# Kernel tuning notes

Measured on AMD Instinct MI355X. Metric: run time of the kernel, lower is better.

Reference implementation:

```python
import jax, jax.numpy as jnp
import numpy as np

EPS = 1e-6  # torch F.pairwise_distance adds eps to the difference


def setup_inputs() -> dict:
    key = jax.random.key(0)
    k1, k2 = jax.random.split(key)
    n_nodes, d = 50000, 512
    n_edges = 150000
    z = jax.random.normal(k1, (n_nodes, d), dtype=jnp.float32)
    edge_index = jax.random.randint(k2, (2, n_edges), 0, n_nodes, dtype=jnp.int64)
    return {"z": z, "edge_index": edge_index}


def reference(z, edge_index):
    # gather endpoint embeddings: [n_edges, d]
    a = z[edge_index[0]]
    b = z[edge_index[1]]
    # row-normalize to unit L2 norm (matches _norm_batch)
    a = a / jnp.linalg.norm(a, axis=1, keepdims=True)
    b = b / jnp.linalg.norm(b, axis=1, keepdims=True)
    # pairwise L2 distance with torch's eps offset
    diff = a - b + EPS
    distance = jnp.sqrt(jnp.sum(diff * diff, axis=1))
    value = 1.0 - distance
    return jax.nn.sigmoid(value)
```

## Files before the change

### kernel.cpp

```cpp
#include <hip/hip_runtime.h>
#include <hip/hip_fp16.h>
#include <hip/hip_fp8.h>
#include <math.h>

#define EPS 1e-6f

typedef float floatx2_t __attribute__((ext_vector_type(2)));

template <bool HI>
static __device__ __forceinline__ unsigned int pack2_fp8(float a, float b,
                                                         unsigned int old) {
#if __has_builtin(__builtin_amdgcn_cvt_pk_fp8_f32)
    return (unsigned int)__builtin_amdgcn_cvt_pk_fp8_f32(a, b, (int)old, HI);
#else
    __hip_fp8x2_e4m3 h(float2{a, b});
    unsigned int v = (unsigned int)h.__x;
    return HI ? ((old & 0x0000FFFFu) | (v << 16)) : ((old & 0xFFFF0000u) | v);
#endif
}

template <bool HI>
static __device__ __forceinline__ float2 unpack2_fp8(unsigned int w) {
#if __has_builtin(__builtin_amdgcn_cvt_pk_f32_fp8)
    floatx2_t f = __builtin_amdgcn_cvt_pk_f32_fp8((int)w, HI);
    return make_float2(f.x, f.y);
#else
    __hip_fp8x2_e4m3 h;
    h.__x = (__hip_fp8x2_storage_t)(HI ? (w >> 16) : (w & 0xFFFFu));
    float2 r = (float2)h;
    return r;
#endif
}

__global__ __launch_bounds__(256) void prep_fp8_kernel(
    const float* __restrict__ z, unsigned int* __restrict__ zq, int n_nodes) {
    const int lane = threadIdx.x & 63;
    const int wid = (blockIdx.x * 256 + threadIdx.x) >> 6;
    const int n0 = wid * 2;
    const int n1 = n0 + 1;
    if (n0 >= n_nodes) return;
    const bool has1 = (n1 < n_nodes);

    const float4* r0 = (const float4*)(z + (size_t)n0 * 512);
    const float4* r1 = (const float4*)(z + (size_t)(has1 ? n1 : n0) * 512);
    float4 p0 = r0[lane];
    float4 q0 = r0[lane + 64];
    float4 p1 = r1[lane];
    float4 q1 = r1[lane + 64];

    float s2a = p0.x*p0.x + p0.y*p0.y + p0.z*p0.z + p0.w*p0.w
              + q0.x*q0.x + q0.y*q0.y + q0.z*q0.z + q0.w*q0.w;
    float s2b = p1.x*p1.x + p1.y*p1.y + p1.z*p1.z + p1.w*p1.w
              + q1.x*q1.x + q1.y*q1.y + q1.z*q1.z + q1.w*q1.w;

    #pragma unroll
    for (int off = 32; off > 0; off >>= 1) {
        s2a += __shfl_xor(s2a, off, 64);
        s2b += __shfl_xor(s2b, off, 64);
    }
    const float rna = 1.0f / sqrtf(s2a);
    const float rnb = 1.0f / sqrtf(s2b);

    {
        unsigned int u0 = pack2_fp8<false>(p0.x * rna, p0.y * rna, 0u);
        u0 = pack2_fp8<true>(p0.z * rna, p0.w * rna, u0);
        unsigned int u1 = pack2_fp8<false>(q0.x * rna, q0.y * rna, 0u);
        u1 = pack2_fp8<true>(q0.z * rna, q0.w * rna, u1);
        ((uint2*)(zq + (size_t)n0 * 128))[lane] = make_uint2(u0, u1);
    }
    if (has1) {
        unsigned int u0 = pack2_fp8<false>(p1.x * rnb, p1.y * rnb, 0u);
        u0 = pack2_fp8<true>(p1.z * rnb, p1.w * rnb, u0);
        unsigned int u1 = pack2_fp8<false>(q1.x * rnb, q1.y * rnb, 0u);
        u1 = pack2_fp8<true>(q1.z * rnb, q1.w * rnb, u1);
        ((uint2*)(zq + (size_t)n1 * 128))[lane] = make_uint2(u0, u1);
    }
}

__global__ __launch_bounds__(256) void edge_fp8_kernel(
    const unsigned int* __restrict__ zq, const int* __restrict__ edge_index,
    float* __restrict__ out, int n_edges) {
    const int lane = threadIdx.x & 63;
    const int wid = (blockIdx.x * 256 + threadIdx.x) >> 6;
    const int e0 = wid * 4;
    if (e0 >= n_edges) return;
    const int valid = min(n_edges - e0, 4);

    int s[4], d[4];
    #pragma unroll
    for (int k = 0; k < 4; ++k) {
        int e = e0 + ((k < valid) ? k : 0);
        s[k] = edge_index[e];
        d[k] = edge_index[e + n_edges];
    }

    uint2 av[4], bv[4];
    #pragma unroll
    for (int k = 0; k < 4; ++k) {
        av[k] = ((const uint2*)(zq + (size_t)s[k] * 128))[lane];
        bv[k] = ((const uint2*)(zq + (size_t)d[k] * 128))[lane];
    }

    float dot[4];
    #pragma unroll
    for (int k = 0; k < 4; ++k) {
        float2 a01 = unpack2_fp8<false>(av[k].x);
        float2 a23 = unpack2_fp8<true>(av[k].x);
        float2 a45 = unpack2_fp8<false>(av[k].y);
        float2 a67 = unpack2_fp8<true>(av[k].y);
        float2 b01 = unpack2_fp8<false>(bv[k].x);
        float2 b23 = unpack2_fp8<true>(bv[k].x);
        float2 b45 = unpack2_fp8<false>(bv[k].y);
        float2 b67 = unpack2_fp8<true>(bv[k].y);
        float t = fmaf(a01.x, b01.x, 0.0f);
        t = fmaf(a01.y, b01.y, t);
        t = fmaf(a23.x, b23.x, t);
        t = fmaf(a23.y, b23.y, t);
        t = fmaf(a45.x, b45.x, t);
        t = fmaf(a45.y, b45.y, t);
        t = fmaf(a67.x, b67.x, t);
        t = fmaf(a67.y, b67.y, t);
        dot[k] = t;
    }

    #pragma unroll
    for (int off = 32; off > 0; off >>= 1) {
        #pragma unroll
        for (int k = 0; k < 4; ++k) dot[k] += __shfl_xor(dot[k], off, 64);
    }

    if (lane == 0) {
        const float self_val = 1.0f - sqrtf(512.0f) * EPS;
        float o[4];
        #pragma unroll
        for (int k = 0; k < 4; ++k) {
            float v;
            if (s[k] == d[k]) {
                v = self_val;
            } else {
                float t = fmaxf(2.0f - 2.0f * dot[k], 0.0f);
                v = 1.0f - sqrtf(t);
            }
            o[k] = 1.0f / (1.0f + expf(-v));
        }
        if (valid == 4) {
            ((float4*)(out + e0))[0] = make_float4(o[0], o[1], o[2], o[3]);
        } else {
            for (int k = 0; k < valid; ++k) out[e0 + k] = o[k];
        }
    }
}

__global__ __launch_bounds__(256) void node_rnorm_kernel(
    const float* __restrict__ z, float* __restrict__ rnorm, int n_nodes) {
    const int lane = threadIdx.x & 63;
    const int node = blockIdx.x * 4 + (threadIdx.x >> 6);
    if (node >= n_nodes) return;
    const float4* row = (const float4*)(z + (size_t)node * 512);
    float4 p = row[lane];
    float4 q = row[lane + 64];
    float s = p.x*p.x + p.y*p.y + p.z*p.z + p.w*p.w
            + q.x*q.x + q.y*q.y + q.z*q.z + q.w*q.w;
    #pragma unroll
    for (int off = 32; off > 0; off >>= 1) s += __shfl_down(s, off, 64);
    if (lane == 0) rnorm[node] = 1.0f / sqrtf(s);
}

__global__ __launch_bounds__(256) void edge_dist_kernel(
    const float* __restrict__ z, const int* __restrict__ edge_index,
    const float* __restrict__ rnorm, float* __restrict__ out, int n_edges) {
    const int lane = threadIdx.x & 63;
    const int edge = blockIdx.x * 4 + (threadIdx.x >> 6);
    if (edge >= n_edges) return;
    const int src = edge_index[edge];
    const int dst = edge_index[edge + n_edges];
    const float rna = rnorm[src];
    const float rnb = rnorm[dst];
    const float4* ra = (const float4*)(z + (size_t)src * 512);
    const float4* rb = (const float4*)(z + (size_t)dst * 512);
    float4 a0 = ra[lane];
    float4 b0 = rb[lane];
    float4 a1 = ra[lane + 64];
    float4 b1 = rb[lane + 64];
    float sacc = 0.0f;
    #define ACC(ac, bc) { float dv = (ac) * rna - (bc) * rnb + EPS; sacc = fmaf(dv, dv, sacc); }
    ACC(a0.x, b0.x) ACC(a0.y, b0.y) ACC(a0.z, b0.z) ACC(a0.w, b0.w)
    ACC(a1.x, b1.x) ACC(a1.y, b1.y) ACC(a1.z, b1.z) ACC(a1.w, b1.w)
    #undef ACC
    #pragma unroll
    for (int off = 32; off > 0; off >>= 1) sacc += __shfl_down(sacc, off, 64);
    if (lane == 0) {
        float value = 1.0f - sqrtf(sacc);
        out[edge] = 1.0f / (1.0f + expf(-value));
    }
}

extern "C" void kernel_launch(void* const* d_in, const int* in_sizes, int n_in,
                              void* d_out, int out_size, void* d_ws, size_t ws_size,
                              hipStream_t stream) {
    const float* z = (const float*)d_in[0];
    const int* edge_index = (const int*)d_in[1];
    float* out = (float*)d_out;

    const int n_nodes = in_sizes[0] / 512;
    const int n_edges = in_sizes[1] / 2;

    const size_t zq_bytes = (size_t)n_nodes * 512;

    if (ws_size >= zq_bytes) {
        unsigned int* zq = (unsigned int*)d_ws;
        {
            int waves = (n_nodes + 1) / 2;
            int blocks = (waves + 3) / 4;
            prep_fp8_kernel<<<blocks, 256, 0, stream>>>(z, zq, n_nodes);
        }
        {
            int waves = (n_edges + 3) / 4;
            int blocks = (waves + 3) / 4;
            edge_fp8_kernel<<<blocks, 256, 0, stream>>>(zq, edge_index, out, n_edges);
        }
    } else {
        float* rnorm = (float*)d_ws;
        {
            int blocks = (n_nodes + 3) / 4;
            node_rnorm_kernel<<<blocks, 256, 0, stream>>>(z, rnorm, n_nodes);
        }
        {
            int blocks = (n_edges + 3) / 4;
            edge_dist_kernel<<<blocks, 256, 0, stream>>>(z, edge_index, rnorm, out, n_edges);
        }
    }
}
```

Before: 172.1 us.

## Process eight edges per wavefront with 8-lane groups and 16-byte fp8 loads

The edge kernel now assigns an 8-lane group to each edge, so one wavefront handles eight edges. Each lane issues four 16-byte loads per endpoint row instead of one 8-byte load, and the reduction needs only three shuffle steps. The prep kernel handles four nodes per wavefront instead of two, which gives more memory parallelism per wave. The cost is more registers per lane and smaller contiguous chunks per row access.

```diff
diff --git a/kernel.cpp b/kernel.cpp
--- a/kernel.cpp
+++ b/kernel.cpp
@@ -32,48 +32,61 @@
 #endif
 }
 
+static __device__ __forceinline__ float dot_u4_fp8(uint4 a, uint4 b, float t) {
+    #pragma unroll
+    for (int j = 0; j < 4; ++j) {
+        unsigned int aw = (&a.x)[j];
+        unsigned int bw = (&b.x)[j];
+        float2 alo = unpack2_fp8<false>(aw);
+        float2 ahi = unpack2_fp8<true>(aw);
+        float2 blo = unpack2_fp8<false>(bw);
+        float2 bhi = unpack2_fp8<true>(bw);
+        t = fmaf(alo.x, blo.x, t);
+        t = fmaf(alo.y, blo.y, t);
+        t = fmaf(ahi.x, bhi.x, t);
+        t = fmaf(ahi.y, bhi.y, t);
+    }
+    return t;
+}
+
 __global__ __launch_bounds__(256) void prep_fp8_kernel(
     const float* __restrict__ z, unsigned int* __restrict__ zq, int n_nodes) {
     const int lane = threadIdx.x & 63;
     const int wid = (blockIdx.x * 256 + threadIdx.x) >> 6;
-    const int n0 = wid * 2;
-    const int n1 = n0 + 1;
+    const int n0 = wid * 4;
     if (n0 >= n_nodes) return;
-    const bool has1 = (n1 < n_nodes);
-
-    const float4* r0 = (const float4*)(z + (size_t)n0 * 512);
-    const float4* r1 = (const float4*)(z + (size_t)(has1 ? n1 : n0) * 512);
-    float4 p0 = r0[lane];
-    float4 q0 = r0[lane + 64];
-    float4 p1 = r1[lane];
-    float4 q1 = r1[lane + 64];
-
-    float s2a = p0.x*p0.x + p0.y*p0.y + p0.z*p0.z + p0.w*p0.w
-              + q0.x*q0.x + q0.y*q0.y + q0.z*q0.z + q0.w*q0.w;
-    float s2b = p1.x*p1.x + p1.y*p1.y + p1.z*p1.z + p1.w*p1.w
-              + q1.x*q1.x + q1.y*q1.y + q1.z*q1.z + q1.w*q1.w;
-
+
+    int n[4];
+    float4 p[4], q[4];
+    #pragma unroll
+    for (int k = 0; k < 4; ++k) {
+        n[k] = min(n0 + k, n_nodes - 1);
+        const float4* r = (const float4*)(z + (size_t)n[k] * 512);
+        p[k] = r[lane];
+        q[k] = r[lane + 64];
+    }
+
+    float s2[4];
+    #pragma unroll
+    for (int k = 0; k < 4; ++k) {
+        s2[k] = p[k].x*p[k].x + p[k].y*p[k].y + p[k].z*p[k].z + p[k].w*p[k].w
+              + q[k].x*q[k].x + q[k].y*q[k].y + q[k].z*q[k].z + q[k].w*q[k].w;
+    }
     #pragma unroll
     for (int off = 32; off > 0; off >>= 1) {
-        s2a += __shfl_xor(s2a, off, 64);
-        s2b += __shfl_xor(s2b, off, 64);
-    }
-    const float rna = 1.0f / sqrtf(s2a);
-    const float rnb = 1.0f / sqrtf(s2b);
-
-    {
-        unsigned int u0 = pack2_fp8<false>(p0.x * rna, p0.y * rna, 0u);
-        u0 = pack2_fp8<true>(p0.z * rna, p0.w * rna, u0);
-        unsigned int u1 = pack2_fp8<false>(q0.x * rna, q0.y * rna, 0u);
-        u1 = pack2_fp8<true>(q0.z * rna, q0.w * rna, u1);
-        ((uint2*)(zq + (size_t)n0 * 128))[lane] = make_uint2(u0, u1);
-    }
-    if (has1) {
-        unsigned int u0 = pack2_fp8<false>(p1.x * rnb, p1.y * rnb, 0u);
-        u0 = pack2_fp8<true>(p1.z * rnb, p1.w * rnb, u0);
-        unsigned int u1 = pack2_fp8<false>(q1.x * rnb, q1.y * rnb, 0u);
-        u1 = pack2_fp8<true>(q1.z * rnb, q1.w * rnb, u1);
-        ((uint2*)(zq + (size_t)n1 * 128))[lane] = make_uint2(u0, u1);
+        #pragma unroll
+        for (int k = 0; k < 4; ++k) s2[k] += __shfl_xor(s2[k], off, 64);
+    }
+
+    #pragma unroll
+    for (int k = 0; k < 4; ++k) {
+        if (k > 0 && n0 + k >= n_nodes) break;
+        const float rn = 1.0f / sqrtf(s2[k]);
+        unsigned int u0 = pack2_fp8<false>(p[k].x * rn, p[k].y * rn, 0u);
+        u0 = pack2_fp8<true>(p[k].z * rn, p[k].w * rn, u0);
+        unsigned int u1 = pack2_fp8<false>(q[k].x * rn, q[k].y * rn, 0u);
+        u1 = pack2_fp8<true>(q[k].z * rn, q[k].w * rn, u1);
+        ((uint2*)(zq + (size_t)n[k] * 128))[lane] = make_uint2(u0, u1);
     }
 }
 
@@ -81,73 +94,47 @@
     const unsigned int* __restrict__ zq, const int* __restrict__ edge_index,
     float* __restrict__ out, int n_edges) {
     const int lane = threadIdx.x & 63;
+    const int t = lane & 7;
+    const int g = lane >> 3;
     const int wid = (blockIdx.x * 256 + threadIdx.x) >> 6;
-    const int e0 = wid * 4;
-    if (e0 >= n_edges) return;
-    const int valid = min(n_edges - e0, 4);
-
-    int s[4], d[4];
-    #pragma unroll
-    for (int k = 0; k < 4; ++k) {
-        int e = e0 + ((k < valid) ? k : 0);
-        s[k] = edge_index[e];
-        d[k] = edge_index[e + n_edges];
-    }
-
-    uint2 av[4], bv[4];
-    #pragma unroll
-    for (int k = 0; k < 4; ++k) {
-        av[k] = ((const uint2*)(zq + (size_t)s[k] * 128))[lane];
-        bv[k] = ((const uint2*)(zq + (size_t)d[k] * 128))[lane];
-    }
-
-    float dot[4];
-    #pragma unroll
-    for (int k = 0; k < 4; ++k) {
-        float2 a01 = unpack2_fp8<false>(av[k].x);
-        float2 a23 = unpack2_fp8<true>(av[k].x);
-        float2 a45 = unpack2_fp8<false>(av[k].y);
-        float2 a67 = unpack2_fp8<true>(av[k].y);
-        float2 b01 = unpack2_fp8<false>(bv[k].x);
-        float2 b23 = unpack2_fp8<true>(bv[k].x);
-        float2 b45 = unpack2_fp8<false>(bv[k].y);
-        float2 b67 = unpack2_fp8<true>(bv[k].y);
-        float t = fmaf(a01.x, b01.x, 0.0f);
-        t = fmaf(a01.y, b01.y, t);
-        t = fmaf(a23.x, b23.x, t);
-        t = fmaf(a23.y, b23.y, t);
-        t = fmaf(a45.x, b45.x, t);
-        t = fmaf(a45.y, b45.y, t);
-        t = fmaf(a67.x, b67.x, t);
-        t = fmaf(a67.y, b67.y, t);
-        dot[k] = t;
-    }
-
-    #pragma unroll
-    for (int off = 32; off > 0; off >>= 1) {
-        #pragma unroll
-        for (int k = 0; k < 4; ++k) dot[k] += __shfl_xor(dot[k], off, 64);
-    }
-
-    if (lane == 0) {
-        const float self_val = 1.0f - sqrtf(512.0f) * EPS;
-        float o[4];
-        #pragma unroll
-        for (int k = 0; k < 4; ++k) {
-            float v;
-            if (s[k] == d[k]) {
-                v = self_val;
-            } else {
-                float t = fmaxf(2.0f - 2.0f * dot[k], 0.0f);
-                v = 1.0f - sqrtf(t);
-            }
-            o[k] = 1.0f / (1.0f + expf(-v));
-        }
-        if (valid == 4) {
-            ((float4*)(out + e0))[0] = make_float4(o[0], o[1], o[2], o[3]);
+    const int e = wid * 8 + g;
+    if (wid * 8 >= n_edges) return;
+    const int ec = min(e, n_edges - 1);
+
+    const int s = edge_index[ec];
+    const int d = edge_index[ec + n_edges];
+
+    const uint4* ra = (const uint4*)(zq + (size_t)s * 128);
+    const uint4* rb = (const uint4*)(zq + (size_t)d * 128);
+
+    uint4 a0 = ra[t];
+    uint4 a1 = ra[t + 8];
+    uint4 a2 = ra[t + 16];
+    uint4 a3 = ra[t + 24];
+    uint4 b0 = rb[t];
+    uint4 b1 = rb[t + 8];
+    uint4 b2 = rb[t + 16];
+    uint4 b3 = rb[t + 24];
+
+    float dot = 0.0f;
+    dot = dot_u4_fp8(a0, b0, dot);
+    dot = dot_u4_fp8(a1, b1, dot);
+    dot = dot_u4_fp8(a2, b2, dot);
+    dot = dot_u4_fp8(a3, b3, dot);
+
+    dot += __shfl_xor(dot, 1, 64);
+    dot += __shfl_xor(dot, 2, 64);
+    dot += __shfl_xor(dot, 4, 64);
+
+    if (t == 0 && e < n_edges) {
+        float v;
+        if (s == d) {
+            v = 1.0f - sqrtf(512.0f) * EPS;
         } else {
-            for (int k = 0; k < valid; ++k) out[e0 + k] = o[k];
-        }
+            float tt = fmaxf(2.0f - 2.0f * dot, 0.0f);
+            v = 1.0f - sqrtf(tt);
+        }
+        out[e] = 1.0f / (1.0f + expf(-v));
     }
 }
 
@@ -210,12 +197,12 @@
     if (ws_size >= zq_bytes) {
         unsigned int* zq = (unsigned int*)d_ws;
         {
-            int waves = (n_nodes + 1) / 2;
+            int waves = (n_nodes + 3) / 4;
             int blocks = (waves + 3) / 4;
             prep_fp8_kernel<<<blocks, 256, 0, stream>>>(z, zq, n_nodes);
         }
         {
-            int waves = (n_edges + 3) / 4;
+            int waves = (n_edges + 7) / 8;
             int blocks = (waves + 3) / 4;
             edge_fp8_kernel<<<blocks, 256, 0, stream>>>(zq, edge_index, out, n_edges);
         }
```

Result: no change. 171.5 us (-0.3%).
